# Kernel optimization log

Measured on AMD Instinct MI355X. Metric: run time of the kernel, lower is better.

The kernel has to match this reference:

```python
import jax, jax.numpy as jnp
import numpy as np

CELL = 8
POS_MARGIN = 1.0
NEG_MARGIN = 0.2
LAMBDA_D = 250.0
LAMBDA_LOSS = 0.0001


def _resize_bilinear(x, out_h, out_w):
    # torch F.interpolate(..., mode='bilinear', align_corners=False) half-pixel sampling
    B, H, W = x.shape
    def axis(n_in, n_out):
        src = (jnp.arange(n_out, dtype=jnp.float32) + 0.5) * (n_in / n_out) - 0.5
        src = jnp.clip(src, 0.0, n_in - 1.0)
        i0 = jnp.floor(src).astype(jnp.int32)
        i1 = jnp.minimum(i0 + 1, n_in - 1)
        w = src - i0.astype(jnp.float32)
        return i0, i1, w
    r0, r1, wr = axis(H, out_h)
    xr = x[:, r0, :] * (1.0 - wr)[None, :, None] + x[:, r1, :] * wr[None, :, None]
    c0, c1, wc = axis(W, out_w)
    return xr[:, :, c0] * (1.0 - wc)[None, None, :] + xr[:, :, c1] * wc[None, None, :]


def detector_loss(pred, heatmap, vm):
    eps = 1e-7
    pos_inds = (heatmap == 1.0).astype(pred.dtype)
    neg_inds = (heatmap < 1.0).astype(pred.dtype)
    neg_weights = (1.0 - heatmap) ** 4
    num_pos = pos_inds.sum()
    pos_loss = (jnp.log(pred + eps) * (1.0 - pred) ** 2 * pos_inds * vm).sum()
    neg_loss = (jnp.log(1.0 - pred + eps) * pred ** 2 * neg_weights * neg_inds * vm).sum()
    return jnp.where(num_pos == 0, -neg_loss, -(pos_loss + neg_loss) / jnp.maximum(num_pos, 1.0))


def descriptor_loss(desc, wdesc, Hmat, vm, wvm):
    B, D, Hc, Wc = desc.shape
    N = Hc * Wc
    # cell-center coordinates in (row=y, col=x) order
    ii, jj = np.meshgrid(np.arange(Hc), np.arange(Wc), indexing='ij')
    coords = (np.stack([ii, jj], axis=-1) * CELL + CELL // 2).astype(np.float32)  # [Hc,Wc,2]
    coords = jnp.asarray(coords)
    pts = coords.reshape(-1, 2)
    # warp points with homographies (convert (y,x) -> (x,y), apply H, convert back)
    H_list = Hmat[:, 0]  # [B,3,3]
    homog = jnp.concatenate([pts[:, ::-1], jnp.ones((N, 1), jnp.float32)], axis=-1)  # [N,3]
    w = jnp.einsum('bij,nj->bni', H_list, homog)
    warped = (w[..., :2] / w[..., 2:3])[..., ::-1]  # back to (y,x), [B,N,2]
    warped = warped.reshape(B, Hc, Wc, 1, 1, 2)
    cell_dist = jnp.linalg.norm(coords.reshape(1, 1, 1, Hc, Wc, 2) - warped, axis=-1)  # [B,Hc,Wc,Hc,Wc]
    s = (cell_dist <= CELL - 0.5).astype(jnp.float32)

    normalization = wvm.sum()
    vm_c = _resize_bilinear(vm, Hc, Wc) > 0.5
    wvm_c = _resize_bilinear(wvm, Hc, Wc) > 0.5
    valid_pair = (vm_c.reshape(B, Hc, Wc, 1, 1) & wvm_c.reshape(B, 1, 1, Hc, Wc)).astype(jnp.float32)

    def l2norm(x):
        return x / jnp.maximum(jnp.linalg.norm(x, axis=-1, keepdims=True), 1e-12)

    d = l2norm(jnp.transpose(desc, (0, 2, 3, 1)))    # [B,Hc,Wc,D]
    wd = l2norm(jnp.transpose(wdesc, (0, 2, 3, 1)))  # [B,Hc,Wc,D]
    dot = jnp.einsum('bijd,bkld->bijkl', d, wd)      # all-pairs cosine sim
    dot = jax.nn.relu(dot)
    positive_dist = jnp.maximum(0.0, POS_MARGIN - dot)
    negative_dist = jnp.maximum(0.0, dot - NEG_MARGIN)
    loss = (LAMBDA_D * s * positive_dist + (1.0 - s) * negative_dist) * valid_pair
    return loss.sum() / normalization


def setup_inputs() -> dict:
    key = jax.random.key(0)
    ks = jax.random.split(key, 8)
    B, H, W, D, Hc, Wc = 2, 480, 640, 256, 60, 80
    Hmat = jnp.eye(3, dtype=jnp.float32)[None, None] + 0.05 * jax.random.normal(ks[6], (B, 1, 3, 3), jnp.float32)
    return {
        'prob': jax.random.uniform(ks[0], (B, H, W), jnp.float32),
        'ht': jax.random.uniform(ks[1], (B, H, W), jnp.float32),
        'valid_mask': jnp.ones((B, H, W), jnp.float32),
        'warped_prob': jax.random.uniform(ks[2], (B, H, W), jnp.float32),
        'warped_ht': jax.random.uniform(ks[3], (B, H, W), jnp.float32),
        'warped_valid_mask': jnp.ones((B, H, W), jnp.float32),
        'desc_raw': jax.random.normal(ks[4], (B, D, Hc, Wc), jnp.float32),
        'warped_desc_raw': jax.random.normal(ks[5], (B, D, Hc, Wc), jnp.float32),
        'Hmat': Hmat,
    }


def reference(prob, ht, valid_mask, warped_prob, warped_ht, warped_valid_mask, desc_raw, warped_desc_raw, Hmat):
    points_loss = detector_loss(prob, ht, valid_mask)
    warped_points_loss = detector_loss(warped_prob, warped_ht, warped_valid_mask)
    desc_loss = descriptor_loss(desc_raw, warped_desc_raw, Hmat, valid_mask, warped_valid_mask)
    total = points_loss + warped_points_loss + LAMBDA_LOSS * desc_loss
    return total, points_loss, warped_points_loss, desc_loss
```

## Files before the change

### kernel.cpp

```cpp
#include <hip/hip_runtime.h>
#include <hip/hip_bf16.h>
#include <cmath>

#define BB 2
#define HH 480
#define WW 640
#define DD 256
#define HC 60
#define WC 80
#define NN (HC*WC)

#define DET_BLOCKS 300
#define SUMSQ_NB ((NN + 255)/256)
#define GEOM_NB ((BB*NN + 255)/256)
#define P1_BLOCKS (16*SUMSQ_NB + GEOM_NB)

#define NTILES64 (NN/64)
#define DESC_BLOCKS_F32 (BB*NTILES64*NTILES64)
#define TS3 96
#define BK 32
#define NT96 (NN/TS3)
#define BLK96 (NT96*NT96)
#define GEMM_BLOCKS (BB*BLK96)
#define CORR_BLOCKS (BB*NN/4)
#define DET_ROLE_BLOCKS (2*DET_BLOCKS)
#define DESC_PARTIALS (GEMM_BLOCKS + CORR_BLOCKS)
#define DESC_GRID (DESC_PARTIALS + DET_ROLE_BLOCKS)

#define OFF_DET0  0
#define OFF_DET1  2048
#define OFF_INVA  16384
#define OFF_INVB  (OFF_INVA + BB*NN)
#define OFF_WRW   (OFF_INVB + BB*NN)
#define OFF_WCL   (OFF_WRW + BB*NN)
#define OFF_VMC   (OFF_WCL + BB*NN)
#define OFF_WVMC  (OFF_VMC + BB*NN)
#define OFF_SQP   (OFF_WVMC + BB*NN)
#define OFF_DESCP (OFF_SQP + 16*NN)
#define OFF_TA    172032
#define TA_FLOATS (BB*NN*DD/2)
#define OFF_TB    (OFF_TA + TA_FLOATS)
#define WS_NEED   ((size_t)(OFF_TB + TA_FLOATS) * 4)

typedef __attribute__((ext_vector_type(8))) short short8;
typedef __attribute__((ext_vector_type(4))) float f32x4;

__device__ inline float bf2f(unsigned short u)
{
    unsigned int x = ((unsigned int)u) << 16;
    return __builtin_bit_cast(float, x);
}

__device__ inline void det_accum(float p, float h, float v,
                                 float& posl, float& negl, float& npos, float& vsum)
{
    float omp = 1.f - p;
    if (h == 1.0f) {
        posl += __logf(p + 1e-7f) * omp*omp * v;
        npos += 1.f;
    }
    if (h < 1.0f) {
        float oh = 1.f - h;
        float w4 = oh*oh; w4 *= w4;
        negl += __logf(omp + 1e-7f) * p*p * w4 * v;
    }
    vsum += v;
}

__device__ inline void det_role(
    int set, int db, int tid,
    const float* __restrict__ pred0, const float* __restrict__ hmap0, const float* __restrict__ vm0,
    const float* __restrict__ pred1, const float* __restrict__ hmap1, const float* __restrict__ vm1,
    float* __restrict__ ws, float* __restrict__ red)
{
    const float4* pred = (const float4*)(set ? pred1 : pred0);
    const float4* hmap = (const float4*)(set ? hmap1 : hmap0);
    const float4* vm   = (const float4*)(set ? vm1   : vm0);
    float* partials = ws + (set ? OFF_DET1 : OFF_DET0);

    float posl = 0.f, negl = 0.f, npos = 0.f, vsum = 0.f;
    const int total4 = BB*HH*WW/4;
    for (int i = db*256 + tid; i < total4; i += DET_BLOCKS*256) {
        float4 p = pred[i], h = hmap[i], v = vm[i];
        det_accum(p.x, h.x, v.x, posl, negl, npos, vsum);
        det_accum(p.y, h.y, v.y, posl, negl, npos, vsum);
        det_accum(p.z, h.z, v.z, posl, negl, npos, vsum);
        det_accum(p.w, h.w, v.w, posl, negl, npos, vsum);
    }
    float vals[4] = {posl, negl, npos, vsum};
    for (int j = 0; j < 4; ++j) {
        red[tid] = vals[j]; __syncthreads();
        for (int s = 128; s > 0; s >>= 1) { if (tid < s) red[tid] += red[tid+s]; __syncthreads(); }
        if (tid == 0) partials[db*4 + j] = red[0];
        __syncthreads();
    }
}

__device__ inline float bilin_cell(const float* __restrict__ x, int i, int j)
{
    float sr = (i + 0.5f) * ((float)HH/(float)HC) - 0.5f;
    sr = fminf(fmaxf(sr, 0.f), (float)(HH-1));
    int r0 = (int)floorf(sr); int r1 = min(r0+1, HH-1); float wr = sr - (float)r0;
    float sc = (j + 0.5f) * ((float)WW/(float)WC) - 0.5f;
    sc = fminf(fmaxf(sc, 0.f), (float)(WW-1));
    int c0 = (int)floorf(sc); int c1 = min(c0+1, WW-1); float wc = sc - (float)c0;
    float v00 = x[r0*WW+c0], v01 = x[r0*WW+c1];
    float v10 = x[r1*WW+c0], v11 = x[r1*WW+c1];
    float e0 = v00*(1.f-wr) + v10*wr;
    float e1 = v01*(1.f-wr) + v11*wr;
    return e0*(1.f-wc) + e1*wc;
}

__device__ inline void prep_geom(int idx, const float* __restrict__ vm,
                                 const float* __restrict__ wvm,
                                 const float* __restrict__ Hmat, float* __restrict__ ws)
{
    int b = idx / NN, n = idx % NN;
    int i = n / WC, j = n % WC;
    float px = (float)(j*8 + 4), py = (float)(i*8 + 4);
    const float* Hb = Hmat + b*9;
    float w0 = Hb[0]*px + Hb[1]*py + Hb[2];
    float w1 = Hb[3]*px + Hb[4]*py + Hb[5];
    float w2 = Hb[6]*px + Hb[7]*py + Hb[8];
    ws[OFF_WRW + idx] = w1 / w2;
    ws[OFF_WCL + idx] = w0 / w2;
    ws[OFF_VMC  + idx] = (bilin_cell(vm  + (size_t)b*HH*WW, i, j) > 0.5f) ? 1.f : 0.f;
    ws[OFF_WVMC + idx] = (bilin_cell(wvm + (size_t)b*HH*WW, i, j) > 0.5f) ? 1.f : 0.f;
}

__global__ __launch_bounds__(256) void phase1_kernel(
    const float* __restrict__ desc, const float* __restrict__ wdesc,
    const float* __restrict__ vm, const float* __restrict__ wvm,
    const float* __restrict__ Hmat, float* __restrict__ ws)
{
    const int bidx = blockIdx.x;
    if (bidx < 16*SUMSQ_NB) {
        const int combo = bidx / SUMSQ_NB;
        const int nb    = bidx % SUMSQ_NB;
        const int z  = combo >> 2;
        const int dc = combo & 3;
        const int n  = nb*256 + threadIdx.x;
        if (n >= NN) return;
        const float* src = ((z & 1) ? wdesc : desc) + (size_t)(z >> 1)*DD*NN;
        float s = 0.f;
        const int d0 = dc*64;
        #pragma unroll 8
        for (int d = d0; d < d0 + 64; ++d) {
            float v = src[(size_t)d*NN + n];
            s = fmaf(v, v, s);
        }
        ws[OFF_SQP + ((size_t)z*4 + dc)*NN + n] = s;
        return;
    }
    const int idx = (bidx - 16*SUMSQ_NB)*256 + threadIdx.x;
    if (idx >= BB*NN) return;
    prep_geom(idx, vm, wvm, Hmat, ws);
}

__global__ __launch_bounds__(256) void prep_kernel_full(
    const float* __restrict__ desc, const float* __restrict__ wdesc,
    const float* __restrict__ vm, const float* __restrict__ wvm,
    const float* __restrict__ Hmat, float* __restrict__ ws)
{
    int idx = blockIdx.x*256 + threadIdx.x;
    if (idx >= BB*NN) return;
    int b = idx / NN, n = idx % NN;

    const float* a  = desc  + (size_t)b*DD*NN + n;
    const float* bp = wdesc + (size_t)b*DD*NN + n;
    float sa = 0.f, sb = 0.f;
    for (int d = 0; d < DD; ++d) {
        float x = a[(size_t)d*NN];  sa = fmaf(x, x, sa);
        float y = bp[(size_t)d*NN]; sb = fmaf(y, y, sb);
    }
    ws[OFF_INVA + idx] = 1.f / fmaxf(sqrtf(sa), 1e-12f);
    ws[OFF_INVB + idx] = 1.f / fmaxf(sqrtf(sb), 1e-12f);
    prep_geom(idx, vm, wvm, Hmat, ws);
}

__global__ __launch_bounds__(256) void det_kernel(
    const float* __restrict__ pred0, const float* __restrict__ hmap0, const float* __restrict__ vm0,
    const float* __restrict__ pred1, const float* __restrict__ hmap1, const float* __restrict__ vm1,
    float* __restrict__ ws)
{
    __shared__ float red[256];
    det_role(blockIdx.x / DET_BLOCKS, blockIdx.x % DET_BLOCKS, threadIdx.x,
             pred0, hmap0, vm0, pred1, hmap1, vm1, ws, red);
}

__global__ __launch_bounds__(256) void transpose_kernel(
    const float* __restrict__ desc, const float* __restrict__ wdesc,
    unsigned short* __restrict__ ta, unsigned short* __restrict__ tb,
    const float* __restrict__ ws)
{
    const int nb = blockIdx.x * 64;
    const int db = blockIdx.y * 64;
    const int z  = blockIdx.z;
    const int b  = z >> 1;
    const float* src = (z & 1) ? wdesc : desc;
    unsigned short* dst = (z & 1) ? tb : ta;
    src += (size_t)b*DD*NN;
    dst += (size_t)b*NN*DD;

    __shared__ float tile[64][65];
    const int tr = threadIdx.x >> 6;
    const int tc = threadIdx.x & 63;
    #pragma unroll
    for (int i = 0; i < 16; ++i) {
        int d = db + i*4 + tr;
        tile[i*4 + tr][tc] = src[(size_t)d*NN + nb + tc];
    }
    __syncthreads();
    const int n = nb + tc;
    const int gidx = b*NN + n;
    float ss = 0.f;
    #pragma unroll
    for (int k = 0; k < 4; ++k)
        ss += ws[OFF_SQP + ((size_t)z*4 + k)*NN + n];
    const float inv  = 1.f / fmaxf(sqrtf(ss), 1e-12f);
    const float mask = (z & 1) ? ws[OFF_WVMC + gidx] : ws[OFF_VMC + gidx];
    const float scl  = inv * mask;
    #pragma unroll
    for (int gg = 0; gg < 2; ++gg) {
        int g = tr + gg*4;
        short8 v8;
        #pragma unroll
        for (int j = 0; j < 8; ++j) {
            float v = tile[g*8 + j][tc] * scl;
            __hip_bfloat16 h = __float2bfloat16(v);
            v8[j] = (short)__builtin_bit_cast(unsigned short, h);
        }
        int sg = (db >> 3) + g;
        *(short8*)(dst + ((size_t)sg*NN + nb + tc)*8) = v8;
    }
}

__global__ __launch_bounds__(256) void desc_mfma(
    const unsigned short* __restrict__ ta, const unsigned short* __restrict__ tb,
    const float* __restrict__ pred0, const float* __restrict__ hmap0, const float* __restrict__ vm0,
    const float* __restrict__ pred1, const float* __restrict__ hmap1, const float* __restrict__ vm1,
    const float* __restrict__ ws, float* __restrict__ partials)
{
    __shared__ unsigned short As[3][TS3*BK];
    __shared__ unsigned short Bs[3][TS3*BK];
    __shared__ float corr_red[4];

    const int bidx = blockIdx.x;
    const int tid  = threadIdx.x;
    const int lane = tid & 63;
    const int wid  = tid >> 6;

    if (bidx < DET_ROLE_BLOCKS) {
        float* red = (float*)&As[0][0];
        det_role(bidx / DET_BLOCKS, bidx % DET_BLOCKS, tid,
                 pred0, hmap0, vm0, pred1, hmap1, vm1,
                 (float*)ws, red);
        return;
    }

    if (bidx < DET_ROLE_BLOCKS + CORR_BLOCKS) {
        const int cid = bidx - DET_ROLE_BLOCKS;
        const int idx = cid*4 + wid;
        const int cb  = idx / NN, cn = idx % NN;
        const float wrow = ws[OFF_WRW + idx];
        const float wcol = ws[OFF_WCL + idx];
        const float va   = ws[OFF_VMC + idx];
        const unsigned short* tA = ta + (size_t)cb*NN*DD;
        const unsigned short* tB = tb + (size_t)cb*NN*DD;
        const float* wvmc = ws + OFF_WVMC + cb*NN;

        const int sg = lane >> 1;
        const int e  = (lane & 1) * 4;
        const unsigned short* ap = tA + ((size_t)sg*NN + cn)*8 + e;
        float a0 = bf2f(ap[0]), a1 = bf2f(ap[1]), a2 = bf2f(ap[2]), a3 = bf2f(ap[3]);

        const int ibase = (int)floorf((wrow - 4.f) * 0.125f);
        const int jbase = (int)floorf((wcol - 4.f) * 0.125f);
        float corr = 0.f;
        #pragma unroll
        for (int di = 0; di < 2; ++di) {
            #pragma unroll
            for (int dj = 0; dj < 2; ++dj) {
                int ii = ibase + di, jj = jbase + dj;
                float dr = (float)(ii*8 + 4) - wrow;
                float dc = (float)(jj*8 + 4) - wcol;
                bool ok = (ii >= 0) && (ii < HC) && (jj >= 0) && (jj < WC)
                          && (dr*dr + dc*dc) <= 56.25f;
                if (ok) {
                    int m = ii*WC + jj;
                    const unsigned short* bp = tB + ((size_t)sg*NN + m)*8 + e;
                    float d = a0*bf2f(bp[0]);
                    d = fmaf(a1, bf2f(bp[1]), d);
                    d = fmaf(a2, bf2f(bp[2]), d);
                    d = fmaf(a3, bf2f(bp[3]), d);
                    #pragma unroll
                    for (int off = 1; off < 64; off <<= 1)
                        d += __shfl_xor(d, off, 64);
                    float dotr = fmaxf(d, 0.f);
                    float pos = 250.f * fmaxf(1.f - dotr, 0.f);
                    float neg = fmaxf(d - 0.2f, 0.f);
                    corr += (pos - neg) * va * wvmc[m];
                }
            }
        }
        if (lane == 0) corr_red[wid] = corr;
        __syncthreads();
        if (tid == 0)
            partials[bidx - DET_ROLE_BLOCKS] = corr_red[0] + corr_red[1]
                                             + corr_red[2] + corr_red[3];
        return;
    }

    const int g   = bidx - DET_ROLE_BLOCKS - CORR_BLOCKS;
    const int swz = (g & 7) * (GEMM_BLOCKS/8) + (g >> 3);
    const int b   = swz / BLK96;
    const int rr  = swz % BLK96;
    const int n0  = (rr / NT96) * TS3;
    const int m0  = (rr % NT96) * TS3;

    const unsigned short* tab = ta + (size_t)b*NN*DD;
    const unsigned short* tbb = tb + (size_t)b*NN*DD;

#define STAGE(t_, buf_)                                                          \
    {                                                                            \
        _Pragma("unroll")                                                        \
        for (int c = 0; c < 3; ++c) {                                            \
            int c2 = wid*3 + c;                                                  \
            int cA = (c2 < 6) ? c2 : (c2 - 6);                                   \
            int o  = cA*64 + lane;                                               \
            int s  = o / TS3;                                                    \
            int r  = o - s*TS3;                                                  \
            const unsigned short* gp = (c2 < 6)                                  \
                ? (tab + ((size_t)((t_)*4 + s)*NN + n0 + r)*8)                   \
                : (tbb + ((size_t)((t_)*4 + s)*NN + m0 + r)*8);                  \
            unsigned short* l0 = (c2 < 6) ? &As[buf_][cA*512] : &Bs[buf_][cA*512];\
            __builtin_amdgcn_global_load_lds(                                    \
                (const __attribute__((address_space(1))) void*)gp,               \
                (__attribute__((address_space(3))) void*)l0, 16, 0, 0);          \
        }                                                                        \
    }

    const int wr = wid >> 1, wc = wid & 1;
    const int ln15   = lane & 15;
    const int slot16 = lane >> 4;
    f32x4 acc[3][3] = {};

    STAGE(0, 0);
    STAGE(1, 1);

    #pragma unroll
    for (int t = 0; t < 8; ++t) {
        if (t < 7) asm volatile("s_waitcnt vmcnt(3)" ::: "memory");
        else       asm volatile("s_waitcnt vmcnt(0)" ::: "memory");
        __builtin_amdgcn_s_barrier();
        __builtin_amdgcn_sched_barrier(0);
        if (t < 6) STAGE(t+2, (t+2) % 3);
        const unsigned short* Ab = As[t % 3];
        const unsigned short* Bb = Bs[t % 3];
        short8 af[3], bf[3];
        #pragma unroll
        for (int f = 0; f < 3; ++f) {
            int ra = wr*48 + f*16 + ln15;
            af[f] = *(const short8*)(Ab + (slot16*TS3 + ra)*8);
            int rb = wc*48 + f*16 + ln15;
            bf[f] = *(const short8*)(Bb + (slot16*TS3 + rb)*8);
        }
        __builtin_amdgcn_s_setprio(1);
        #pragma unroll
        for (int fi = 0; fi < 3; ++fi)
            #pragma unroll
            for (int fj = 0; fj < 3; ++fj)
                acc[fi][fj] = __builtin_amdgcn_mfma_f32_16x16x32_bf16(
                    af[fi], bf[fj], acc[fi][fj], 0, 0, 0);
        __builtin_amdgcn_s_setprio(0);
    }

    float sum = 0.f;
    #pragma unroll
    for (int fi = 0; fi < 3; ++fi)
        #pragma unroll
        for (int fj = 0; fj < 3; ++fj)
            #pragma unroll
            for (int reg = 0; reg < 4; ++reg)
                sum += fmaxf(acc[fi][fj][reg] - 0.2f, 0.f);

    float* red = (float*)&As[0][0];
    red[tid] = sum; __syncthreads();
    for (int s = 128; s > 0; s >>= 1) { if (tid < s) red[tid] += red[tid+s]; __syncthreads(); }
    if (tid == 0) partials[bidx - DET_ROLE_BLOCKS] = red[0];
#undef STAGE
}

__global__ __launch_bounds__(256) void desc_kernel(
    const float* __restrict__ desc, const float* __restrict__ wdesc,
    const float* __restrict__ ws, float* __restrict__ partials)
{
    const int b  = blockIdx.z;
    const int n0 = blockIdx.y * 64;
    const int m0 = blockIdx.x * 64;
    const float* A  = desc  + (size_t)b*DD*NN;
    const float* Bm = wdesc + (size_t)b*DD*NN;

    __shared__ float As[32][64];
    __shared__ float Bs[32][64];

    const int tid = threadIdx.x;
    const int tx = tid & 15, ty = tid >> 4;
    float acc[4][4] = {{0.f}};

    for (int k0 = 0; k0 < DD; k0 += 32) {
        #pragma unroll
        for (int l = 0; l < 8; ++l) {
            int e = tid + l*256;
            int kk = e >> 6, nn = e & 63;
            As[kk][nn] = A [(size_t)(k0+kk)*NN + n0 + nn];
            Bs[kk][nn] = Bm[(size_t)(k0+kk)*NN + m0 + nn];
        }
        __syncthreads();
        #pragma unroll
        for (int kk = 0; kk < 32; ++kk) {
            float4 av = *reinterpret_cast<const float4*>(&As[kk][ty*4]);
            float4 bv = *reinterpret_cast<const float4*>(&Bs[kk][tx*4]);
            float a4[4] = {av.x, av.y, av.z, av.w};
            float b4[4] = {bv.x, bv.y, bv.z, bv.w};
            #pragma unroll
            for (int r = 0; r < 4; ++r)
                #pragma unroll
                for (int c = 0; c < 4; ++c)
                    acc[r][c] = fmaf(a4[r], b4[c], acc[r][c]);
        }
        __syncthreads();
    }

    const float* inva = ws + OFF_INVA + b*NN;
    const float* invb = ws + OFF_INVB + b*NN;
    const float* wrp  = ws + OFF_WRW + b*NN;
    const float* wcp  = ws + OFF_WCL + b*NN;
    const float* vmc  = ws + OFF_VMC + b*NN;
    const float* wvmc = ws + OFF_WVMC + b*NN;

    int nb = n0 + ty*4, mb = m0 + tx*4;
    float ia[4], wrv[4], wcv[4], va[4];
    #pragma unroll
    for (int r = 0; r < 4; ++r) {
        int n = nb + r;
        ia[r] = inva[n]; wrv[r] = wrp[n]; wcv[r] = wcp[n]; va[r] = vmc[n];
    }
    float ib[4], vb[4], crow[4], ccol[4];
    #pragma unroll
    for (int c = 0; c < 4; ++c) {
        int m = mb + c;
        ib[c] = invb[m]; vb[c] = wvmc[m];
        crow[c] = (float)((m / WC)*8 + 4);
        ccol[c] = (float)((m % WC)*8 + 4);
    }
    float sum = 0.f;
    #pragma unroll
    for (int r = 0; r < 4; ++r) {
        #pragma unroll
        for (int c = 0; c < 4; ++c) {
            float dot = fmaxf(acc[r][c] * ia[r] * ib[c], 0.f);
            float dr = crow[c] - wrv[r];
            float dc = ccol[c] - wcv[r];
            bool s = (dr*dr + dc*dc) <= 56.25f;
            float term = s ? 250.f * fmaxf(1.f - dot, 0.f)
                           : fmaxf(dot - 0.2f, 0.f);
            sum += term * va[r] * vb[c];
        }
    }

    __shared__ float red[256];
    red[tid] = sum; __syncthreads();
    for (int s = 128; s > 0; s >>= 1) { if (tid < s) red[tid] += red[tid+s]; __syncthreads(); }
    if (tid == 0) {
        int bid = (blockIdx.z * gridDim.y + blockIdx.y) * gridDim.x + blockIdx.x;
        partials[bid] = red[0];
    }
}

__global__ __launch_bounds__(256) void finalize_kernel(
    const float* __restrict__ ws, float* __restrict__ out, int desc_nblocks)
{
    __shared__ float red[256];
    int t = threadIdx.x;
    float res[2];
    float norm = 0.f;
    for (int pass = 0; pass < 2; ++pass) {
        const float* p = ws + (pass == 0 ? OFF_DET0 : OFF_DET1);
        float s0=0.f, s1=0.f, s2=0.f, s3=0.f;
        for (int i = t; i < DET_BLOCKS; i += 256) {
            s0 += p[i*4+0]; s1 += p[i*4+1]; s2 += p[i*4+2]; s3 += p[i*4+3];
        }
        float v[4] = {s0,s1,s2,s3};
        float tot[4];
        for (int j = 0; j < 4; ++j) {
            red[t] = v[j]; __syncthreads();
            for (int s = 128; s > 0; s >>= 1) { if (t < s) red[t] += red[t+s]; __syncthreads(); }
            tot[j] = red[0]; __syncthreads();
        }
        float posl = tot[0], negl = tot[1], npos = tot[2], vsum = tot[3];
        res[pass] = (npos == 0.f) ? -negl : -(posl + negl) / fmaxf(npos, 1.f);
        if (pass == 1) norm = vsum;
    }
    float ds = 0.f;
    for (int i = t; i < desc_nblocks; i += 256) ds += ws[OFF_DESCP + i];
    red[t] = ds; __syncthreads();
    for (int s = 128; s > 0; s >>= 1) { if (t < s) red[t] += red[t+s]; __syncthreads(); }
    float descsum = red[0];
    if (t == 0) {
        float desc_loss = descsum / norm;
        float total = res[0] + res[1] + 1e-4f * desc_loss;
        out[0] = total;
        out[1] = res[0];
        out[2] = res[1];
        out[3] = desc_loss;
    }
}

extern "C" void kernel_launch(void* const* d_in, const int* in_sizes, int n_in,
                              void* d_out, int out_size, void* d_ws, size_t ws_size,
                              hipStream_t stream)
{
    const float* prob  = (const float*)d_in[0];
    const float* htm   = (const float*)d_in[1];
    const float* vmask = (const float*)d_in[2];
    const float* wprob = (const float*)d_in[3];
    const float* wht   = (const float*)d_in[4];
    const float* wvm   = (const float*)d_in[5];
    const float* desc  = (const float*)d_in[6];
    const float* wdesc = (const float*)d_in[7];
    const float* Hm    = (const float*)d_in[8];
    float* ws  = (float*)d_ws;
    float* out = (float*)d_out;

    if (ws_size >= WS_NEED) {
        unsigned short* ta = (unsigned short*)(ws + OFF_TA);
        unsigned short* tb = (unsigned short*)(ws + OFF_TB);
        phase1_kernel<<<P1_BLOCKS, 256, 0, stream>>>(desc, wdesc, vmask, wvm, Hm, ws);
        transpose_kernel<<<dim3(NN/64, DD/64, BB*2), 256, 0, stream>>>(desc, wdesc, ta, tb, ws);
        desc_mfma<<<DESC_GRID, 256, 0, stream>>>(
            ta, tb, prob, htm, vmask, wprob, wht, wvm, ws, ws + OFF_DESCP);
        finalize_kernel<<<1, 256, 0, stream>>>(ws, out, DESC_PARTIALS);
    } else {
        det_kernel<<<2*DET_BLOCKS, 256, 0, stream>>>(
            prob, htm, vmask, wprob, wht, wvm, ws);
        prep_kernel_full<<<(BB*NN + 255)/256, 256, 0, stream>>>(desc, wdesc, vmask, wvm, Hm, ws);
        desc_kernel<<<dim3(NTILES64, NTILES64, BB), 256, 0, stream>>>(desc, wdesc, ws, ws + OFF_DESCP);
        finalize_kernel<<<1, 256, 0, stream>>>(ws, out, DESC_BLOCKS_F32);
    }
}
```

Before: 66.33 us.

## Enlarge MFMA Gram tile to 192x192 with 512-thread blocks

Measured after the change: 57.73 us, median of 2. 1.15x faster.

```diff
diff --git a/kernel.cpp b/kernel.cpp
--- a/kernel.cpp
+++ b/kernel.cpp
@@ -17,12 +17,12 @@
 
 #define NTILES64 (NN/64)
 #define DESC_BLOCKS_F32 (BB*NTILES64*NTILES64)
-#define TS3 96
+#define TS4 192
 #define BK 32
-#define NT96 (NN/TS3)
-#define BLK96 (NT96*NT96)
-#define GEMM_BLOCKS (BB*BLK96)
-#define CORR_BLOCKS (BB*NN/4)
+#define NT192 (NN/TS4)
+#define BLK192 (NT192*NT192)
+#define GEMM_BLOCKS (BB*BLK192)
+#define CORR_BLOCKS (BB*NN/8)
 #define DET_ROLE_BLOCKS (2*DET_BLOCKS)
 #define DESC_PARTIALS (GEMM_BLOCKS + CORR_BLOCKS)
 #define DESC_GRID (DESC_PARTIALS + DET_ROLE_BLOCKS)
@@ -68,7 +68,7 @@
 }
 
 __device__ inline void det_role(
-    int set, int db, int tid,
+    int set, int db, int tid, int nthr,
     const float* __restrict__ pred0, const float* __restrict__ hmap0, const float* __restrict__ vm0,
     const float* __restrict__ pred1, const float* __restrict__ hmap1, const float* __restrict__ vm1,
     float* __restrict__ ws, float* __restrict__ red)
@@ -80,7 +80,7 @@
 
     float posl = 0.f, negl = 0.f, npos = 0.f, vsum = 0.f;
     const int total4 = BB*HH*WW/4;
-    for (int i = db*256 + tid; i < total4; i += DET_BLOCKS*256) {
+    for (int i = db*nthr + tid; i < total4; i += DET_BLOCKS*nthr) {
         float4 p = pred[i], h = hmap[i], v = vm[i];
         det_accum(p.x, h.x, v.x, posl, negl, npos, vsum);
         det_accum(p.y, h.y, v.y, posl, negl, npos, vsum);
@@ -90,7 +90,7 @@
     float vals[4] = {posl, negl, npos, vsum};
     for (int j = 0; j < 4; ++j) {
         red[tid] = vals[j]; __syncthreads();
-        for (int s = 128; s > 0; s >>= 1) { if (tid < s) red[tid] += red[tid+s]; __syncthreads(); }
+        for (int s = nthr >> 1; s > 0; s >>= 1) { if (tid < s) red[tid] += red[tid+s]; __syncthreads(); }
         if (tid == 0) partials[db*4 + j] = red[0];
         __syncthreads();
     }
@@ -184,7 +184,7 @@
     float* __restrict__ ws)
 {
     __shared__ float red[256];
-    det_role(blockIdx.x / DET_BLOCKS, blockIdx.x % DET_BLOCKS, threadIdx.x,
+    det_role(blockIdx.x / DET_BLOCKS, blockIdx.x % DET_BLOCKS, threadIdx.x, 256,
              pred0, hmap0, vm0, pred1, hmap1, vm1, ws, red);
 }
 
@@ -235,15 +235,15 @@
     }
 }
 
-__global__ __launch_bounds__(256) void desc_mfma(
+__global__ __launch_bounds__(512, 4) void desc_mfma(
     const unsigned short* __restrict__ ta, const unsigned short* __restrict__ tb,
     const float* __restrict__ pred0, const float* __restrict__ hmap0, const float* __restrict__ vm0,
     const float* __restrict__ pred1, const float* __restrict__ hmap1, const float* __restrict__ vm1,
     const float* __restrict__ ws, float* __restrict__ partials)
 {
-    __shared__ unsigned short As[3][TS3*BK];
-    __shared__ unsigned short Bs[3][TS3*BK];
-    __shared__ float corr_red[4];
+    __shared__ unsigned short As[3][TS4*BK];
+    __shared__ unsigned short Bs[3][TS4*BK];
+    __shared__ float corr_red[8];
 
     const int bidx = blockIdx.x;
     const int tid  = threadIdx.x;
@@ -252,7 +252,7 @@
 
     if (bidx < DET_ROLE_BLOCKS) {
         float* red = (float*)&As[0][0];
-        det_role(bidx / DET_BLOCKS, bidx % DET_BLOCKS, tid,
+        det_role(bidx / DET_BLOCKS, bidx % DET_BLOCKS, tid, 512,
                  pred0, hmap0, vm0, pred1, hmap1, vm1,
                  (float*)ws, red);
         return;
@@ -260,7 +260,7 @@
 
     if (bidx < DET_ROLE_BLOCKS + CORR_BLOCKS) {
         const int cid = bidx - DET_ROLE_BLOCKS;
-        const int idx = cid*4 + wid;
+        const int idx = cid*8 + wid;
         const int cb  = idx / NN, cn = idx % NN;
         const float wrow = ws[OFF_WRW + idx];
         const float wcol = ws[OFF_WCL + idx];
@@ -305,18 +305,23 @@
         }
         if (lane == 0) corr_red[wid] = corr;
         __syncthreads();
-        if (tid == 0)
-            partials[bidx - DET_ROLE_BLOCKS] = corr_red[0] + corr_red[1]
-                                             + corr_red[2] + corr_red[3];
+        if (tid == 0) {
+            float c = 0.f;
+            #pragma unroll
+            for (int w = 0; w < 8; ++w) c += corr_red[w];
+            partials[bidx - DET_ROLE_BLOCKS] = c;
+        }
         return;
     }
 
-    const int g   = bidx - DET_ROLE_BLOCKS - CORR_BLOCKS;
-    const int swz = (g & 7) * (GEMM_BLOCKS/8) + (g >> 3);
-    const int b   = swz / BLK96;
-    const int rr  = swz % BLK96;
-    const int n0  = (rr / NT96) * TS3;
-    const int m0  = (rr % NT96) * TS3;
+    const int g = bidx - DET_ROLE_BLOCKS - CORR_BLOCKS;
+    const int xcd = g & 7, oi = g >> 3;
+    const int q = GEMM_BLOCKS / 8, r = GEMM_BLOCKS % 8;
+    const int swz = (xcd < r ? xcd*(q+1) : r*(q+1) + (xcd - r)*q) + oi;
+    const int b   = swz / BLK192;
+    const int rr  = swz % BLK192;
+    const int n0  = (rr / NT192) * TS4;
+    const int m0  = (rr % NT192) * TS4;
 
     const unsigned short* tab = ta + (size_t)b*NN*DD;
     const unsigned short* tbb = tb + (size_t)b*NN*DD;
@@ -326,24 +331,25 @@
         _Pragma("unroll")                                                        \
         for (int c = 0; c < 3; ++c) {                                            \
             int c2 = wid*3 + c;                                                  \
-            int cA = (c2 < 6) ? c2 : (c2 - 6);                                   \
+            int cA = (c2 < 12) ? c2 : (c2 - 12);                                 \
             int o  = cA*64 + lane;                                               \
-            int s  = o / TS3;                                                    \
-            int r  = o - s*TS3;                                                  \
-            const unsigned short* gp = (c2 < 6)                                  \
-                ? (tab + ((size_t)((t_)*4 + s)*NN + n0 + r)*8)                   \
-                : (tbb + ((size_t)((t_)*4 + s)*NN + m0 + r)*8);                  \
-            unsigned short* l0 = (c2 < 6) ? &As[buf_][cA*512] : &Bs[buf_][cA*512];\
+            int s  = o / TS4;                                                    \
+            int rr2 = o - s*TS4;                                                 \
+            const unsigned short* gp = (c2 < 12)                                 \
+                ? (tab + ((size_t)((t_)*4 + s)*NN + n0 + rr2)*8)                 \
+                : (tbb + ((size_t)((t_)*4 + s)*NN + m0 + rr2)*8);                \
+            unsigned short* l0 = (c2 < 12) ? &As[buf_][cA*512] : &Bs[buf_][cA*512];\
             __builtin_amdgcn_global_load_lds(                                    \
                 (const __attribute__((address_space(1))) void*)gp,               \
                 (__attribute__((address_space(3))) void*)l0, 16, 0, 0);          \
         }                                                                        \
     }
 
-    const int wr = wid >> 1, wc = wid & 1;
+    const int wr = wid >> 2;
+    const int wc = wid & 3;
     const int ln15   = lane & 15;
     const int slot16 = lane >> 4;
-    f32x4 acc[3][3] = {};
+    f32x4 acc[6][3] = {};
 
     STAGE(0, 0);
     STAGE(1, 1);
@@ -357,17 +363,20 @@
         if (t < 6) STAGE(t+2, (t+2) % 3);
         const unsigned short* Ab = As[t % 3];
         const unsigned short* Bb = Bs[t % 3];
-        short8 af[3], bf[3];
+        short8 af[6], bf[3];
+        #pragma unroll
+        for (int f = 0; f < 6; ++f) {
+            int ra = wr*96 + f*16 + ln15;
+            af[f] = *(const short8*)(Ab + (slot16*TS4 + ra)*8);
+        }
         #pragma unroll
         for (int f = 0; f < 3; ++f) {
-            int ra = wr*48 + f*16 + ln15;
-            af[f] = *(const short8*)(Ab + (slot16*TS3 + ra)*8);
             int rb = wc*48 + f*16 + ln15;
-            bf[f] = *(const short8*)(Bb + (slot16*TS3 + rb)*8);
+            bf[f] = *(const short8*)(Bb + (slot16*TS4 + rb)*8);
         }
         __builtin_amdgcn_s_setprio(1);
         #pragma unroll
-        for (int fi = 0; fi < 3; ++fi)
+        for (int fi = 0; fi < 6; ++fi)
             #pragma unroll
             for (int fj = 0; fj < 3; ++fj)
                 acc[fi][fj] = __builtin_amdgcn_mfma_f32_16x16x32_bf16(
@@ -377,7 +386,7 @@
 
     float sum = 0.f;
     #pragma unroll
-    for (int fi = 0; fi < 3; ++fi)
+    for (int fi = 0; fi < 6; ++fi)
         #pragma unroll
         for (int fj = 0; fj < 3; ++fj)
             #pragma unroll
@@ -386,7 +395,7 @@
 
     float* red = (float*)&As[0][0];
     red[tid] = sum; __syncthreads();
-    for (int s = 128; s > 0; s >>= 1) { if (tid < s) red[tid] += red[tid+s]; __syncthreads(); }
+    for (int s = 256; s > 0; s >>= 1) { if (tid < s) red[tid] += red[tid+s]; __syncthreads(); }
     if (tid == 0) partials[bidx - DET_ROLE_BLOCKS] = red[0];
 #undef STAGE
 }
@@ -538,7 +547,7 @@
         unsigned short* tb = (unsigned short*)(ws + OFF_TB);
         phase1_kernel<<<P1_BLOCKS, 256, 0, stream>>>(desc, wdesc, vmask, wvm, Hm, ws);
         transpose_kernel<<<dim3(NN/64, DD/64, BB*2), 256, 0, stream>>>(desc, wdesc, ta, tb, ws);
-        desc_mfma<<<DESC_GRID, 256, 0, stream>>>(
+        desc_mfma<<<DESC_GRID, 512, 0, stream>>>(
             ta, tb, prob, htm, vmask, wprob, wht, wvm, ws, ws + OFF_DESCP);
         finalize_kernel<<<1, 256, 0, stream>>>(ws, out, DESC_PARTIALS);
     } else {
```
